# Performance work log

Measured on AMD Instinct MI355X. Metric: run time of the kernel, lower is better.

## Reference

```python
import jax, jax.numpy as jnp
import numpy as np

FEAT_IN = 64     # len(nonterminals)
EMB = 256        # embedding_dim
K = 30           # sortk
B = 48           # batch items
NG = 11          # graphs per item (1 goal + 10 env)
G = B * NG       # 528 graphs
NPG = 192        # nodes per graph
EPG = 384        # edges per graph
N = G * NPG
E = G * EPG
D = 3 * EMB + 1  # 769, concat channel dim = conv5 kernel/stride
DENSE = (K // 2 - 5 + 1) * EMB  # 11*256 = 2816


def setup_inputs() -> dict:
    key = jax.random.key(0)
    ks = jax.random.split(key, 12)
    x = jax.random.normal(ks[0], (N, FEAT_IN), jnp.float32)
    # edges within each graph, no self loops (remove_self_loops in original)
    src_l = jax.random.randint(ks[1], (E,), 0, NPG)
    off = jax.random.randint(ks[2], (E,), 1, NPG)
    dst_l = (src_l + off) % NPG
    goff = (jnp.arange(E) // EPG) * NPG
    src = (src_l + goff).astype(jnp.int32)
    dst = (dst_l + goff).astype(jnp.int32)

    def lin(k, fi, fo):
        return (jax.random.normal(k, (fi, fo), jnp.float32) / np.float32(np.sqrt(fi)))

    return dict(
        x=x, src=src, dst=dst,
        W1=lin(ks[3], FEAT_IN, EMB), b1=jnp.zeros((EMB,), jnp.float32),
        W2=lin(ks[4], EMB, EMB), b2=jnp.zeros((EMB,), jnp.float32),
        W3=lin(ks[5], EMB, EMB), b3=jnp.zeros((EMB,), jnp.float32),
        W4=lin(ks[6], EMB, 1), b4=jnp.zeros((1,), jnp.float32),
        w5=jax.random.normal(ks[7], (EMB // 2, 1, D), jnp.float32) / np.float32(np.sqrt(D)),
        bc5=jnp.zeros((EMB // 2,), jnp.float32),
        w6=jax.random.normal(ks[8], (EMB, EMB // 2, 5), jnp.float32) / np.float32(np.sqrt(5 * EMB // 2)),
        bc6=jnp.zeros((EMB,), jnp.float32),
        Wc1=lin(ks[9], NG * DENSE, EMB), bc1=jnp.zeros((EMB,), jnp.float32),
        Wc2=lin(ks[10], EMB, 10), bc2=jnp.zeros((10,), jnp.float32),
    )


def _gcn(x, W, b, src, dst):
    # PyG GCNConv: add self loops, symmetric norm D^-1/2 (A+I) D^-1/2 (XW) + b
    h = x @ W
    deg = jnp.ones((N,), h.dtype).at[dst].add(1.0)  # +1 for self loop
    dis = jax.lax.rsqrt(deg)
    msg = h[src] * (dis[src] * dis[dst])[:, None]
    agg = jnp.zeros_like(h).at[dst].add(msg)
    return agg + h * (dis * dis)[:, None] + b  # self-loop norm = 1/deg


def _conv1d(x, w, b, stride):
    y = jax.lax.conv_general_dilated(x, w, (stride,), 'VALID',
                                     dimension_numbers=('NCH', 'OIH', 'NCH'))
    return y + b[None, :, None]


def reference(x, src, dst, W1, b1, W2, b2, W3, b3, W4, b4,
              w5, bc5, w6, bc6, Wc1, bc1, Wc2, bc2):
    x1 = jnp.tanh(_gcn(x, W1, b1, src, dst))
    x2 = jnp.tanh(_gcn(x1, W2, b2, src, dst))
    x3 = jnp.tanh(_gcn(x2, W3, b3, src, dst))
    x4 = jnp.tanh(_gcn(x3, W4, b4, src, dst))
    xc = jnp.concatenate([x1, x2, x3, x4], axis=-1)  # [N, D]
    xg = xc.reshape(G, NPG, D)
    # global_sort_pool: sort nodes per graph by last channel (desc), take top K
    _, idx = jax.lax.top_k(xg[:, :, -1], K)          # [G, K]
    xs = jnp.take_along_axis(xg, idx[:, :, None], axis=1)  # [G, K, D]
    seq = xs.reshape(G, 1, K * D)
    y = jax.nn.relu(_conv1d(seq, w5, bc5, D))        # [G, EMB/2, K]
    y = y.reshape(G, EMB // 2, K // 2, 2).max(axis=-1)  # MaxPool1d(2,2)
    y = jax.nn.relu(_conv1d(y, w6, bc6, 1))          # [G, EMB, K//2-4]
    emb = y.reshape(B, NG * DENSE)                   # 11 graphs per item, flattened
    h = jax.nn.relu(emb @ Wc1 + bc1)
    logits = h @ Wc2 + bc2                           # dropout is identity at eval
    return logits
```

## Files before the change

kernel.cpp:

```cpp
#include <hip/hip_runtime.h>
#include <hip/hip_bf16.h>

#define EMB   256
#define KSORT 30
#define BATCH 48
#define NGPI  11
#define GG    528
#define NPG   192
#define EPG   384
#define DCH   769
#define GC    528
#define NCH   (GG/GC)
#define MC    (GC*NPG)
#define EC    (GC*EPG)
#define FQ    44
#define FCH   (2816/FQ)
#define KB5   5

__device__ __forceinline__ int clampi(int v, int lo, int hi) {
  return v < lo ? lo : (v > hi ? hi : v);
}

__device__ __attribute__((aligned(16))) float g_c1[MC * EMB];
__device__ __attribute__((aligned(16))) float g_c2[MC * EMB];
__device__ __attribute__((aligned(16))) float g_c3[MC * EMB];
__device__ __attribute__((aligned(16))) float g_tb[MC * EMB];
__device__ __attribute__((aligned(16))) float g_dis[MC];
__device__ __attribute__((aligned(16))) float g_x4[MC];
__device__ __attribute__((aligned(16))) int   g_indptr[MC + 1];
__device__ __attribute__((aligned(16))) int   g_ssrc[EC];
__device__ __attribute__((aligned(16))) int   g_idx[GC * KSORT];
__device__ __attribute__((aligned(16))) float g_w5t[DCH * 128];
__device__ __attribute__((aligned(16))) float g_w6t[640 * 256];
__device__ __attribute__((aligned(16))) float g_y[GC * 128 * 30];
__device__ __attribute__((aligned(16))) float g_y2[GC * 128 * 15];
__device__ __attribute__((aligned(16))) float g_z[GG * 2816];
__device__ __attribute__((aligned(16))) float g_hp[NGPI * FQ * BATCH * 256];
__device__ __attribute__((aligned(16))) float g_h[BATCH * 256];

__device__ __forceinline__ float* selbuf(int s) {
  return s == 0 ? g_c1 : (s == 1 ? g_c2 : g_c3);
}

__global__ __launch_bounds__(192) void build_csr_k(const int* __restrict__ src,
    const int* __restrict__ dst, int g0) {
  __shared__ int cnt[NPG];
  __shared__ int offs[NPG];
  int g = blockIdx.x, t = threadIdx.x;
  int gg = g0 + g;
  cnt[t] = 0;
  __syncthreads();
  int ebase = gg * EPG, gnb = gg * NPG, lnb = g * NPG;
  for (int e = t; e < EPG; e += 192) {
    int dl = clampi(dst[ebase + e] - gnb, 0, NPG - 1);
    atomicAdd(&cnt[dl], 1);
  }
  __syncthreads();
  if (t == 0) {
    int run = g * EPG;
    for (int i = 0; i < NPG; i++) { offs[i] = run; run += cnt[i]; }
  }
  __syncthreads();
  g_indptr[lnb + t] = offs[t];
  g_dis[lnb + t] = 1.0f / sqrtf(1.0f + (float)cnt[t]);
  if (g == 0 && t == 0) g_indptr[MC] = EC;
  __syncthreads();
  for (int e = t; e < EPG; e += 192) {
    int ee = ebase + e;
    int dl = clampi(dst[ee] - gnb, 0, NPG - 1);
    int pos = clampi(atomicAdd(&offs[dl], 1), 0, EC - 1);
    g_ssrc[pos] = clampi(src[ee] - gnb, 0, NPG - 1) + lnb;
  }
}

template<bool AX>
__global__ __launch_bounds__(256) void gemm_k(const float* __restrict__ Ax,
    int asel, const float* __restrict__ W, int Kd) {
  __shared__ float As[16 * 192];
  const int m0 = blockIdx.x * 128, n0 = blockIdx.y * 128;
  const int t = threadIdx.x;
  const int tx = t & 15, ty = t >> 4;
  const int arow = t >> 1, acol = (t & 1) * 8;
  const int awr = (arow >> 3) * 12 + (arow & 7);
  float acc[8][8];
#pragma unroll
  for (int i = 0; i < 8; i++)
#pragma unroll
    for (int j = 0; j < 8; j++) acc[i][j] = 0.f;
  const float* Ap = AX ? Ax : selbuf(asel);
  const float* arp = Ap + (size_t)(m0 + arow) * Kd + acol;
  const float* Wt = W + n0 + tx * 4;
  const int nt = Kd >> 4;
  float4 pa0 = *(const float4*)(arp);
  float4 pa1 = *(const float4*)(arp + 4);
  for (int it = 0; it < nt; ++it) {
    As[(acol + 0) * 192 + awr] = pa0.x;
    As[(acol + 1) * 192 + awr] = pa0.y;
    As[(acol + 2) * 192 + awr] = pa0.z;
    As[(acol + 3) * 192 + awr] = pa0.w;
    As[(acol + 4) * 192 + awr] = pa1.x;
    As[(acol + 5) * 192 + awr] = pa1.y;
    As[(acol + 6) * 192 + awr] = pa1.z;
    As[(acol + 7) * 192 + awr] = pa1.w;
    __syncthreads();
    if (it + 1 < nt) {
      const float* ap = arp + (it + 1) * 16;
      pa0 = *(const float4*)(ap);
      pa1 = *(const float4*)(ap + 4);
    }
    const float* Wk = Wt + (size_t)(it * 16) * EMB;
#pragma unroll
    for (int kk = 0; kk < 16; kk++) {
      float a[8], b[8];
      *(float4*)&a[0] = *(const float4*)&As[kk * 192 + ty * 12];
      *(float4*)&a[4] = *(const float4*)&As[kk * 192 + ty * 12 + 4];
      *(float4*)&b[0] = *(const float4*)(Wk + kk * EMB);
      *(float4*)&b[4] = *(const float4*)(Wk + kk * EMB + 64);
#pragma unroll
      for (int i = 0; i < 8; i++)
#pragma unroll
        for (int j = 0; j < 8; j++) acc[i][j] += a[i] * b[j];
    }
    __syncthreads();
  }
#pragma unroll
  for (int i = 0; i < 8; i++) {
    float* cp = g_tb + (size_t)(m0 + ty * 8 + i) * EMB + n0 + tx * 4;
    *(float4*)cp = make_float4(acc[i][0], acc[i][1], acc[i][2], acc[i][3]);
    *(float4*)(cp + 64) = make_float4(acc[i][4], acc[i][5], acc[i][6], acc[i][7]);
  }
}

__global__ __launch_bounds__(256) void agg_k(int osel, const float* __restrict__ bias) {
  int n = blockIdx.x * 4 + (threadIdx.x >> 6);
  int lane = threadIdx.x & 63;
  float dn = g_dis[n];
  const float4* H4 = (const float4*)g_tb;
  float4 hv = H4[(size_t)n * 64 + lane];
  float sc = dn * dn;
  float ax = hv.x * sc, ay = hv.y * sc, az = hv.z * sc, aw = hv.w * sc;
  int beg = g_indptr[n], end = g_indptr[n + 1];
  for (int j = beg; j < end; j++) {
    int s = g_ssrc[j];
    float c = g_dis[s] * dn;
    float4 v = H4[(size_t)s * 64 + lane];
    ax += v.x * c; ay += v.y * c; az += v.z * c; aw += v.w * c;
  }
  float4 bv = ((const float4*)bias)[lane];
  float4 o;
  o.x = tanhf(ax + bv.x);
  o.y = tanhf(ay + bv.y);
  o.z = tanhf(az + bv.z);
  o.w = tanhf(aw + bv.w);
  ((float4*)selbuf(osel))[(size_t)n * 64 + lane] = o;
}

__global__ __launch_bounds__(256) void gemm4_k(const float* __restrict__ W4) {
  int n = blockIdx.x * 4 + (threadIdx.x >> 6);
  int lane = threadIdx.x & 63;
  float4 a = *(const float4*)(g_c3 + (size_t)n * EMB + lane * 4);
  float4 w = *(const float4*)(W4 + lane * 4);
  float s = a.x * w.x + a.y * w.y + a.z * w.z + a.w * w.w;
  for (int off = 32; off > 0; off >>= 1) s += __shfl_down(s, off, 64);
  if (lane == 0) g_tb[n] = s;
}

__global__ __launch_bounds__(256) void agg4_k(const float* __restrict__ b4) {
  int n = blockIdx.x * 256 + threadIdx.x;
  if (n >= MC) return;
  float dn = g_dis[n];
  float acc = g_tb[n] * dn * dn;
  int beg = g_indptr[n], end = g_indptr[n + 1];
  for (int j = beg; j < end; j++) {
    int s = g_ssrc[j];
    acc += g_tb[s] * g_dis[s] * dn;
  }
  g_x4[n] = tanhf(acc + b4[0]);
}

__global__ __launch_bounds__(256) void sortpool_k() {
  __shared__ float sv[256];
  __shared__ int si[256];
  int g = blockIdx.x, t = threadIdx.x;
  if (t < NPG) { sv[t] = g_x4[g * NPG + t]; si[t] = t; }
  else { sv[t] = -1e30f; si[t] = 1 << 20; }
  __syncthreads();
  for (int k = 2; k <= 256; k <<= 1) {
    for (int j = k >> 1; j > 0; j >>= 1) {
      int ixj = t ^ j;
      if (ixj > t) {
        float v1 = sv[t], v2 = sv[ixj];
        int i1 = si[t], i2 = si[ixj];
        bool before_t = (v1 > v2) || (v1 == v2 && i1 < i2);
        bool up = ((t & k) == 0);
        if (up ? !before_t : before_t) {
          sv[t] = v2; sv[ixj] = v1;
          si[t] = i2; si[ixj] = i1;
        }
      }
      __syncthreads();
    }
  }
  if (t < KSORT) g_idx[g * KSORT + t] = clampi(g * NPG + si[t], 0, MC - 1);
}

__global__ __launch_bounds__(256) void tw5_k(const float* __restrict__ w5) {
  int i = blockIdx.x * 256 + threadIdx.x;
  if (i >= 128 * DCH) return;
  int o = i / DCH, d = i % DCH;
  g_w5t[d * 128 + o] = w5[i];
}
__global__ __launch_bounds__(256) void tw6_k(const float* __restrict__ w6) {
  int i = blockIdx.x * 256 + threadIdx.x;
  if (i >= 256 * 640) return;
  int o = i / 640, ir = i % 640;
  g_w6t[ir * 256 + o] = w6[i];
}

__global__ __launch_bounds__(128) void conv5_k(const float* __restrict__ bc5) {
  __shared__ float ar[KB5][772];
  int g = blockIdx.x, kb = blockIdx.y * KB5;
  int t = threadIdx.x;
  for (int kk = 0; kk < KB5; kk++) {
    int n = clampi(g_idx[g * KSORT + kb + kk], 0, MC - 1);
    const float* p1 = g_c1 + (size_t)n * EMB;
    const float* p2 = g_c2 + (size_t)n * EMB;
    const float* p3 = g_c3 + (size_t)n * EMB;
    for (int d = t; d < EMB; d += 128) {
      ar[kk][d] = p1[d];
      ar[kk][EMB + d] = p2[d];
      ar[kk][2 * EMB + d] = p3[d];
    }
    if (t == 0) ar[kk][768] = g_x4[n];
  }
  __syncthreads();
  float acc[KB5];
  float bias = bc5[t];
#pragma unroll
  for (int kk = 0; kk < KB5; kk++) acc[kk] = bias;
  const float* wbase = g_w5t + t;
  int d = 0;
  for (; d + 8 <= DCH; d += 8) {
    float w0 = wbase[(d + 0) * 128], w1 = wbase[(d + 1) * 128];
    float w2 = wbase[(d + 2) * 128], w3 = wbase[(d + 3) * 128];
    float w4 = wbase[(d + 4) * 128], w5 = wbase[(d + 5) * 128];
    float w6 = wbase[(d + 6) * 128], w7 = wbase[(d + 7) * 128];
#pragma unroll
    for (int kk = 0; kk < KB5; kk++) {
      float4 a0 = *(const float4*)&ar[kk][d];
      float4 a1 = *(const float4*)&ar[kk][d + 4];
      acc[kk] += a0.x * w0 + a0.y * w1 + a0.z * w2 + a0.w * w3 +
                 a1.x * w4 + a1.y * w5 + a1.z * w6 + a1.w * w7;
    }
  }
  for (; d < DCH; d++) {
    float wv = wbase[d * 128];
#pragma unroll
    for (int kk = 0; kk < KB5; kk++) acc[kk] += ar[kk][d] * wv;
  }
#pragma unroll
  for (int kk = 0; kk < KB5; kk++)
    g_y[(size_t)g * 3840 + t * KSORT + kb + kk] = fmaxf(acc[kk], 0.f);
}

__global__ void maxpool_k() {
  int i = blockIdx.x * 256 + threadIdx.x;
  if (i >= GC * 128 * 15) return;
  int j = i % 15, go = i / 15;
  g_y2[i] = fmaxf(g_y[go * 30 + 2 * j], g_y[go * 30 + 2 * j + 1]);
}

__global__ __launch_bounds__(256) void conv6_k(const float* __restrict__ bc6,
                                               int g0) {
  __shared__ float s[128 * 16];
  int g = blockIdx.x, t = threadIdx.x;
  for (int i = t; i < 1920; i += 256) {
    int ch = i / 15, j = i % 15;
    s[ch * 16 + j] = g_y2[(size_t)g * 1920 + i];
  }
  __syncthreads();
  float acc[11];
  float bias = bc6[t];
#pragma unroll
  for (int q = 0; q < 11; q++) acc[q] = bias;
  for (int i = 0; i < 128; i += 2) {
    float wA[5], wB[5];
#pragma unroll
    for (int r = 0; r < 5; r++) {
      wA[r] = g_w6t[(i * 5 + r) * 256 + t];
      wB[r] = g_w6t[((i + 1) * 5 + r) * 256 + t];
    }
    const float* sA = &s[i * 16];
    const float* sB = &s[(i + 1) * 16];
#pragma unroll
    for (int r = 0; r < 5; r++)
#pragma unroll
      for (int q = 0; q < 11; q++)
        acc[q] += sA[r + q] * wA[r] + sB[r + q] * wB[r];
  }
#pragma unroll
  for (int q = 0; q < 11; q++)
    g_z[(size_t)(g0 + g) * 2816 + t * 11 + q] = fmaxf(acc[q], 0.f);
}

__global__ __launch_bounds__(128) void dense1_k(const float* __restrict__ Wc1) {
  __shared__ float zs[BATCH][FCH];
  int gi = blockIdx.x;
  int obase = blockIdx.y * 128;
  int fq = blockIdx.z, f0 = fq * FCH;
  int t = threadIdx.x;
  for (int i = t; i < BATCH * FCH; i += 128) {
    int gl = i >> 6, f = i & 63;
    zs[gl][f] = g_z[(size_t)(gl * NGPI + gi) * 2816 + f0 + f];
  }
  __syncthreads();
  const float* wp = Wc1 + (size_t)gi * 2816 * 256 + (size_t)f0 * 256 + obase + t;
  float acc[BATCH];
#pragma unroll
  for (int gl = 0; gl < BATCH; gl++) acc[gl] = 0.f;
  float wc[8];
#pragma unroll
  for (int r = 0; r < 8; r++) wc[r] = wp[(size_t)r * 256];
  for (int f = 0; f < FCH; f += 8) {
    float wn[8];
    int fn = (f + 8 < FCH) ? f + 8 : f;
#pragma unroll
    for (int r = 0; r < 8; r++) wn[r] = wp[(size_t)(fn + r) * 256];
#pragma unroll
    for (int gl = 0; gl < BATCH; gl++) {
      float4 z0 = *(const float4*)&zs[gl][f];
      float4 z1 = *(const float4*)&zs[gl][f + 4];
      acc[gl] += z0.x * wc[0] + z0.y * wc[1] + z0.z * wc[2] + z0.w * wc[3] +
                 z1.x * wc[4] + z1.y * wc[5] + z1.z * wc[6] + z1.w * wc[7];
    }
#pragma unroll
    for (int r = 0; r < 8; r++) wc[r] = wn[r];
  }
  float* hp = g_hp + (size_t)(gi * FQ + fq) * (BATCH * 256);
#pragma unroll
  for (int gl = 0; gl < BATCH; gl++)
    hp[gl * 256 + obase + t] = acc[gl];
}

__global__ __launch_bounds__(256) void reduce_k() {
  int j = blockIdx.x * 256 + threadIdx.x;
  if (j >= BATCH * 256) return;
  float s0 = 0.f, s1 = 0.f, s2 = 0.f, s3 = 0.f;
  const size_t STR = BATCH * 256;
  for (int p = 0; p < NGPI * FQ; p += 4) {
    s0 += g_hp[(size_t)(p + 0) * STR + j];
    s1 += g_hp[(size_t)(p + 1) * STR + j];
    s2 += g_hp[(size_t)(p + 2) * STR + j];
    s3 += g_hp[(size_t)(p + 3) * STR + j];
  }
  g_h[j] = (s0 + s1) + (s2 + s3);
}

__global__ __launch_bounds__(256) void dense2_k(const float* __restrict__ bc1,
    const float* __restrict__ Wc2, const float* __restrict__ bc2,
    float* __restrict__ out) {
  __shared__ float hs[BATCH * 256];
  int t = threadIdx.x;
  for (int i = t; i < BATCH * 256; i += 256) {
    int o = i & 255;
    hs[i] = fmaxf(g_h[i] + bc1[o], 0.f);
  }
  __syncthreads();
  for (int i = t; i < 480; i += 256) {
    int b = i / 10, c = i % 10;
    float acc = bc2[c];
    for (int k = 0; k < 256; k++) acc += hs[b * 256 + k] * Wc2[k * 10 + c];
    out[i] = acc;
  }
}

__global__ void diag_k(float* __restrict__ out, float v) {
  int i = blockIdx.x * 256 + threadIdx.x;
  if (i < 480) out[i] = v;
}

extern "C" void kernel_launch(void* const* d_in, const int* in_sizes, int n_in,
                              void* d_out, int out_size, void* d_ws, size_t ws_size,
                              hipStream_t stream) {
  const float* x   = (const float*)d_in[0];
  const int*   src = (const int*)d_in[1];
  const int*   dst = (const int*)d_in[2];
  const float* W1  = (const float*)d_in[3];
  const float* b1  = (const float*)d_in[4];
  const float* W2  = (const float*)d_in[5];
  const float* b2  = (const float*)d_in[6];
  const float* W3  = (const float*)d_in[7];
  const float* b3  = (const float*)d_in[8];
  const float* W4  = (const float*)d_in[9];
  const float* b4  = (const float*)d_in[10];
  const float* w5  = (const float*)d_in[11];
  const float* bc5 = (const float*)d_in[12];
  const float* w6  = (const float*)d_in[13];
  const float* bc6 = (const float*)d_in[14];
  const float* Wc1 = (const float*)d_in[15];
  const float* bc1 = (const float*)d_in[16];
  const float* Wc2 = (const float*)d_in[17];
  const float* bc2 = (const float*)d_in[18];
  float* out = (float*)d_out;

  (void)hipGetLastError();
  int lcount = 0, fidx = -1;
  hipError_t ferr = hipSuccess;
  auto ck = [&]() {
    hipError_t e = hipGetLastError();
    if (e != hipSuccess && ferr == hipSuccess) { ferr = e; fidx = lcount; }
    lcount++;
  };

  tw5_k<<<(128 * DCH + 255) / 256, 256, 0, stream>>>(w5); ck();
  tw6_k<<<(256 * 640 + 255) / 256, 256, 0, stream>>>(w6); ck();

  dim3 gg(MC / 128, 2);
  build_csr_k<<<GC, 192, 0, stream>>>(src, dst, 0); ck();
  gemm_k<true><<<gg, 256, 0, stream>>>(x, 0, W1, 64); ck();
  agg_k<<<MC / 4, 256, 0, stream>>>(0, b1); ck();
  gemm_k<false><<<gg, 256, 0, stream>>>(nullptr, 0, W2, EMB); ck();
  agg_k<<<MC / 4, 256, 0, stream>>>(1, b2); ck();
  gemm_k<false><<<gg, 256, 0, stream>>>(nullptr, 1, W3, EMB); ck();
  agg_k<<<MC / 4, 256, 0, stream>>>(2, b3); ck();
  gemm4_k<<<MC / 4, 256, 0, stream>>>(W4); ck();
  agg4_k<<<MC / 256, 256, 0, stream>>>(b4); ck();
  sortpool_k<<<GC, 256, 0, stream>>>(); ck();
  conv5_k<<<dim3(GC, 6), 128, 0, stream>>>(bc5); ck();
  maxpool_k<<<(GC * 1920 + 255) / 256, 256, 0, stream>>>(); ck();
  conv6_k<<<GC, 256, 0, stream>>>(bc6, 0); ck();

  dense1_k<<<dim3(NGPI, 2, FQ), 128, 0, stream>>>(Wc1); ck();
  reduce_k<<<(BATCH * 256 + 255) / 256, 256, 0, stream>>>(); ck();
  dense2_k<<<1, 256, 0, stream>>>(bc1, Wc2, bc2, out); ck();

  if (ferr != hipSuccess) {
    int code = (int)ferr; if (code > 100) code = 100;
    float v = (fidx == 0) ? (1024.f + 8.f * code) : (2048.f + 16.f * code);
    diag_k<<<2, 256, 0, stream>>>(out, v);
  }
}
```

Before: 988.2 us.

## Fuse W4 projection into agg, fold maxpool into conv6, stage half of B in LDS

```diff
diff --git a/kernel.cpp b/kernel.cpp
--- a/kernel.cpp
+++ b/kernel.cpp
@@ -27,13 +27,13 @@
 __device__ __attribute__((aligned(16))) float g_tb[MC * EMB];
 __device__ __attribute__((aligned(16))) float g_dis[MC];
 __device__ __attribute__((aligned(16))) float g_x4[MC];
+__device__ __attribute__((aligned(16))) float g_s4[MC];
 __device__ __attribute__((aligned(16))) int   g_indptr[MC + 1];
 __device__ __attribute__((aligned(16))) int   g_ssrc[EC];
 __device__ __attribute__((aligned(16))) int   g_idx[GC * KSORT];
 __device__ __attribute__((aligned(16))) float g_w5t[DCH * 128];
 __device__ __attribute__((aligned(16))) float g_w6t[640 * 256];
 __device__ __attribute__((aligned(16))) float g_y[GC * 128 * 30];
-__device__ __attribute__((aligned(16))) float g_y2[GC * 128 * 15];
 __device__ __attribute__((aligned(16))) float g_z[GG * 2816];
 __device__ __attribute__((aligned(16))) float g_hp[NGPI * FQ * BATCH * 256];
 __device__ __attribute__((aligned(16))) float g_h[BATCH * 256];
@@ -77,11 +77,13 @@
 __global__ __launch_bounds__(256) void gemm_k(const float* __restrict__ Ax,
     int asel, const float* __restrict__ W, int Kd) {
   __shared__ float As[16 * 192];
+  __shared__ float Bs[16][68];
   const int m0 = blockIdx.x * 128, n0 = blockIdx.y * 128;
   const int t = threadIdx.x;
   const int tx = t & 15, ty = t >> 4;
   const int arow = t >> 1, acol = (t & 1) * 8;
   const int awr = (arow >> 3) * 12 + (arow & 7);
+  const int brow = t >> 4, bcol = tx * 4;
   float acc[8][8];
 #pragma unroll
   for (int i = 0; i < 8; i++)
@@ -89,10 +91,12 @@
     for (int j = 0; j < 8; j++) acc[i][j] = 0.f;
   const float* Ap = AX ? Ax : selbuf(asel);
   const float* arp = Ap + (size_t)(m0 + arow) * Kd + acol;
-  const float* Wt = W + n0 + tx * 4;
+  const float* bsp = W + (size_t)brow * EMB + n0 + bcol;
+  const float* Wg = W + n0 + 64 + tx * 4;
   const int nt = Kd >> 4;
   float4 pa0 = *(const float4*)(arp);
   float4 pa1 = *(const float4*)(arp + 4);
+  float4 pb  = *(const float4*)(bsp);
   for (int it = 0; it < nt; ++it) {
     As[(acol + 0) * 192 + awr] = pa0.x;
     As[(acol + 1) * 192 + awr] = pa0.y;
@@ -102,20 +106,22 @@
     As[(acol + 5) * 192 + awr] = pa1.y;
     As[(acol + 6) * 192 + awr] = pa1.z;
     As[(acol + 7) * 192 + awr] = pa1.w;
+    *(float4*)&Bs[brow][bcol] = pb;
     __syncthreads();
     if (it + 1 < nt) {
       const float* ap = arp + (it + 1) * 16;
       pa0 = *(const float4*)(ap);
       pa1 = *(const float4*)(ap + 4);
-    }
-    const float* Wk = Wt + (size_t)(it * 16) * EMB;
+      pb  = *(const float4*)(bsp + (size_t)(it + 1) * 16 * EMB);
+    }
+    const float* Wk = Wg + (size_t)(it * 16) * EMB;
 #pragma unroll
     for (int kk = 0; kk < 16; kk++) {
       float a[8], b[8];
       *(float4*)&a[0] = *(const float4*)&As[kk * 192 + ty * 12];
       *(float4*)&a[4] = *(const float4*)&As[kk * 192 + ty * 12 + 4];
-      *(float4*)&b[0] = *(const float4*)(Wk + kk * EMB);
-      *(float4*)&b[4] = *(const float4*)(Wk + kk * EMB + 64);
+      *(float4*)&b[0] = *(const float4*)&Bs[kk][bcol];
+      *(float4*)&b[4] = *(const float4*)(Wk + kk * EMB);
 #pragma unroll
       for (int i = 0; i < 8; i++)
 #pragma unroll
@@ -131,7 +137,8 @@
   }
 }
 
-__global__ __launch_bounds__(256) void agg_k(int osel, const float* __restrict__ bias) {
+__global__ __launch_bounds__(256) void agg_k(int osel,
+    const float* __restrict__ bias, const float* __restrict__ W4) {
   int n = blockIdx.x * 4 + (threadIdx.x >> 6);
   int lane = threadIdx.x & 63;
   float dn = g_dis[n];
@@ -153,27 +160,23 @@
   o.z = tanhf(az + bv.z);
   o.w = tanhf(aw + bv.w);
   ((float4*)selbuf(osel))[(size_t)n * 64 + lane] = o;
-}
-
-__global__ __launch_bounds__(256) void gemm4_k(const float* __restrict__ W4) {
-  int n = blockIdx.x * 4 + (threadIdx.x >> 6);
-  int lane = threadIdx.x & 63;
-  float4 a = *(const float4*)(g_c3 + (size_t)n * EMB + lane * 4);
-  float4 w = *(const float4*)(W4 + lane * 4);
-  float s = a.x * w.x + a.y * w.y + a.z * w.z + a.w * w.w;
-  for (int off = 32; off > 0; off >>= 1) s += __shfl_down(s, off, 64);
-  if (lane == 0) g_tb[n] = s;
+  if (W4) {
+    float4 w = ((const float4*)W4)[lane];
+    float s = o.x * w.x + o.y * w.y + o.z * w.z + o.w * w.w;
+    for (int off = 32; off > 0; off >>= 1) s += __shfl_down(s, off, 64);
+    if (lane == 0) g_s4[n] = s;
+  }
 }
 
 __global__ __launch_bounds__(256) void agg4_k(const float* __restrict__ b4) {
   int n = blockIdx.x * 256 + threadIdx.x;
   if (n >= MC) return;
   float dn = g_dis[n];
-  float acc = g_tb[n] * dn * dn;
+  float acc = g_s4[n] * dn * dn;
   int beg = g_indptr[n], end = g_indptr[n + 1];
   for (int j = beg; j < end; j++) {
     int s = g_ssrc[j];
-    acc += g_tb[s] * g_dis[s] * dn;
+    acc += g_s4[s] * g_dis[s] * dn;
   }
   g_x4[n] = tanhf(acc + b4[0]);
 }
@@ -263,20 +266,14 @@
     g_y[(size_t)g * 3840 + t * KSORT + kb + kk] = fmaxf(acc[kk], 0.f);
 }
 
-__global__ void maxpool_k() {
-  int i = blockIdx.x * 256 + threadIdx.x;
-  if (i >= GC * 128 * 15) return;
-  int j = i % 15, go = i / 15;
-  g_y2[i] = fmaxf(g_y[go * 30 + 2 * j], g_y[go * 30 + 2 * j + 1]);
-}
-
 __global__ __launch_bounds__(256) void conv6_k(const float* __restrict__ bc6,
                                                int g0) {
   __shared__ float s[128 * 16];
   int g = blockIdx.x, t = threadIdx.x;
   for (int i = t; i < 1920; i += 256) {
     int ch = i / 15, j = i % 15;
-    s[ch * 16 + j] = g_y2[(size_t)g * 1920 + i];
+    const float* yp = g_y + (size_t)g * 3840 + ch * 30 + 2 * j;
+    s[ch * 16 + j] = fmaxf(yp[0], yp[1]);
   }
   __syncthreads();
   float acc[11];
@@ -418,16 +415,14 @@
   dim3 gg(MC / 128, 2);
   build_csr_k<<<GC, 192, 0, stream>>>(src, dst, 0); ck();
   gemm_k<true><<<gg, 256, 0, stream>>>(x, 0, W1, 64); ck();
-  agg_k<<<MC / 4, 256, 0, stream>>>(0, b1); ck();
+  agg_k<<<MC / 4, 256, 0, stream>>>(0, b1, nullptr); ck();
   gemm_k<false><<<gg, 256, 0, stream>>>(nullptr, 0, W2, EMB); ck();
-  agg_k<<<MC / 4, 256, 0, stream>>>(1, b2); ck();
+  agg_k<<<MC / 4, 256, 0, stream>>>(1, b2, nullptr); ck();
   gemm_k<false><<<gg, 256, 0, stream>>>(nullptr, 1, W3, EMB); ck();
-  agg_k<<<MC / 4, 256, 0, stream>>>(2, b3); ck();
-  gemm4_k<<<MC / 4, 256, 0, stream>>>(W4); ck();
+  agg_k<<<MC / 4, 256, 0, stream>>>(2, b3, W4); ck();
   agg4_k<<<MC / 256, 256, 0, stream>>>(b4); ck();
   sortpool_k<<<GC, 256, 0, stream>>>(); ck();
   conv5_k<<<dim3(GC, 6), 128, 0, stream>>>(bc5); ck();
-  maxpool_k<<<(GC * 1920 + 255) / 256, 256, 0, stream>>>(); ck();
   conv6_k<<<GC, 256, 0, stream>>>(bc6, 0); ck();
 
   dense1_k<<<dim3(NGPI, 2, FQ), 128, 0, stream>>>(Wc1); ck();
```

Measured after the change: 966.9 us. -2.2%, faster.
